# Kernel optimization log

Measured on AMD Instinct MI355X. Metric: run time of the kernel, lower is better.

Reference implementation:

```python
import jax, jax.numpy as jnp
import numpy as np

PI = np.pi


def _apply_1q(state, gate, wire, n):
    # state: [B, 2**n] complex64; gate: [2,2] (shared) or [B,2,2] (per-sample)
    # PennyLane convention: wire 0 is the most-significant bit of the state index.
    B = state.shape[0]
    left, right = 2 ** wire, 2 ** (n - wire - 1)
    s = state.reshape(B, left, 2, right)
    if gate.ndim == 2:
        s = jnp.einsum('kl,balr->bakr', gate, s)
    else:
        s = jnp.einsum('bkl,balr->bakr', gate, s)
    return s.reshape(B, -1)


def _apply_cz(state, wire, n):
    # CZ on (wire, wire+1): flip sign of |..11..> amplitudes
    B = state.shape[0]
    left, right = 2 ** wire, 2 ** (n - wire - 2)
    s = state.reshape(B, left, 2, 2, right)
    s = s.at[:, :, 1, 1, :].multiply(-1.0)
    return s.reshape(B, -1)


def _ry_batched(theta):
    # theta: [B] -> [B,2,2] complex RY(theta)
    h = 0.5 * theta
    c, s = jnp.cos(h), jnp.sin(h)
    g = jnp.stack([jnp.stack([c, -s], -1), jnp.stack([s, c], -1)], -2)
    return g.astype(jnp.complex64)


def _rot(phi, theta, omega):
    # Rot = RZ(omega) @ RY(theta) @ RZ(phi)
    c, s = jnp.cos(0.5 * theta), jnp.sin(0.5 * theta)
    e_mm = jnp.exp(-0.5j * (phi + omega))
    e_pm = jnp.exp(0.5j * (phi - omega))
    e_mp = jnp.exp(-0.5j * (phi - omega))
    e_pp = jnp.exp(0.5j * (phi + omega))
    g = jnp.stack([jnp.stack([e_mm * c, -e_pm * s]), jnp.stack([e_mp * s, e_pp * c])])
    return g.astype(jnp.complex64)


def _simulate(enc, weights):
    # enc: [B, n_qubits] in [-1,1]; weights: [n_layers, n_qubits, 3]
    n_layers, n, _ = weights.shape
    B = enc.shape[0]
    state = jnp.zeros((B, 2 ** n), jnp.complex64).at[:, 0].set(1.0)
    ry = [_ry_batched(enc[:, i] * PI) for i in range(n)]
    for l in range(n_layers):
        for i in range(n):
            state = _apply_1q(state, ry[i], i, n)
        for i in range(n):
            state = _apply_1q(state, _rot(weights[l, i, 0], weights[l, i, 1], weights[l, i, 2]), i, n)
        for i in range(n - 1):
            state = _apply_cz(state, i, n)
    for i in range(n):
        state = _apply_1q(state, ry[i], i, n)
    probs = state.real ** 2 + state.imag ** 2  # [B, 2**n]
    # <Z_i> = sum_k probs[k] * (-1)^bit_i(k), wire 0 = MSB
    bits = (jnp.arange(2 ** n)[None, :] >> (n - 1 - jnp.arange(n))[:, None]) & 1
    signs = (1 - 2 * bits).astype(probs.dtype)  # [n, 2**n]
    return probs @ signs.T  # [B, n]


def setup_inputs() -> dict:
    B, D, NQ, NL, NA = 32768, 16, 8, 4, 4
    key = jax.random.key(0)
    ks = jax.random.split(key, 6)

    def lin(k, o, i):
        b = 1.0 / np.sqrt(i)
        k1, k2 = jax.random.split(k)
        return (jax.random.uniform(k1, (o, i), jnp.float32, -b, b),
                jax.random.uniform(k2, (o,), jnp.float32, -b, b))

    enc_w1, enc_b1 = lin(ks[1], 8, D)
    enc_w2, enc_b2 = lin(ks[2], NQ, 8)
    dec_w1, dec_b1 = lin(ks[3], 8, NQ)
    dec_w2, dec_b2 = lin(ks[4], NA, 8)
    q_weights = jax.random.uniform(ks[5], (NL, NQ, 3), jnp.float32, 0.0, 2.0 * PI)
    x = jax.random.normal(ks[0], (B, D), jnp.float32)
    return {"x": x, "enc_w1": enc_w1, "enc_b1": enc_b1, "enc_w2": enc_w2, "enc_b2": enc_b2,
            "q_weights": q_weights, "dec_w1": dec_w1, "dec_b1": dec_b1, "dec_w2": dec_w2, "dec_b2": dec_b2}


def reference(x, enc_w1, enc_b1, enc_w2, enc_b2, q_weights, dec_w1, dec_b1, dec_w2, dec_b2):
    h = jax.nn.relu(x @ enc_w1.T + enc_b1)
    enc = jnp.tanh(h @ enc_w2.T + enc_b2)          # [B, n_qubits]
    q = _simulate(enc, q_weights)                  # [B, n_qubits] PauliZ expvals
    h2 = jax.nn.relu(q @ dec_w1.T + dec_b1)
    return h2 @ dec_w2.T + dec_b2                  # [B, n_actions]
```

## Files before the change

kernel.cpp:

```cpp
#include <hip/hip_runtime.h>
#include <math.h>


#define PI_F 3.14159265358979323846f

typedef float v2f __attribute__((ext_vector_type(2)));

struct C2 { float re, im; };
__device__ __forceinline__ C2 cmul(C2 a, C2 b) {
    C2 r;
    r.re = fmaf(a.re, b.re, -a.im * b.im);
    r.im = fmaf(a.re, b.im,  a.im * b.re);
    return r;
}
__device__ __forceinline__ float fxor(float x, int m) {
    return __int_as_float(__float_as_int(x) ^ m);
}

__device__ __forceinline__ v2f pk_mul(v2f a, v2f b) {
    v2f d; asm("v_pk_mul_f32 %0, %1, %2" : "=v"(d) : "v"(a), "v"(b)); return d;
}
__device__ __forceinline__ v2f pk_mul_neg(v2f a, v2f b) {
    v2f d; asm("v_pk_mul_f32 %0, %1, %2 neg_lo:[1,0] neg_hi:[1,0]"
               : "=v"(d) : "v"(a), "v"(b)); return d;
}
__device__ __forceinline__ v2f pk_fma(v2f a, v2f b, v2f c) {
    v2f d; asm("v_pk_fma_f32 %0, %1, %2, %3" : "=v"(d) : "v"(a), "v"(b), "v"(c)); return d;
}
__device__ __forceinline__ v2f pk_fma_nn(v2f a, v2f b, v2f c) {
    v2f d; asm("v_pk_fma_f32 %0, %1, %2, %3 neg_lo:[1,0,0] neg_hi:[1,0,0]"
               : "=v"(d) : "v"(a), "v"(b), "v"(c)); return d;
}
__device__ __forceinline__ v2f pk_fma_swl(v2f a, v2f b, v2f c) {
    v2f d; asm("v_pk_fma_f32 %0, %1, %2, %3 op_sel:[0,1,0] op_sel_hi:[1,0,1] neg_lo:[1,0,0]"
               : "=v"(d) : "v"(a), "v"(b), "v"(c)); return d;
}
__device__ __forceinline__ v2f pk_fma_swh(v2f a, v2f b, v2f c) {
    v2f d; asm("v_pk_fma_f32 %0, %1, %2, %3 op_sel:[0,1,0] op_sel_hi:[1,0,1] neg_hi:[1,0,0]"
               : "=v"(d) : "v"(a), "v"(b), "v"(c)); return d;
}
__device__ __forceinline__ v2f cmulv(v2f z, C2 c) {
    v2f n = pk_mul((v2f){c.re, c.re}, z);
    return pk_fma_swl((v2f){c.im, c.im}, z, n);
}

template<int CTRL>
__device__ __forceinline__ float dppf(float x) {
    int xi = __float_as_int(x);
    int r = __builtin_amdgcn_update_dpp(xi, xi, CTRL, 0xF, 0xF, false);
    return __int_as_float(r);
}
template<int M>
__device__ __forceinline__ float lxor(float x) {
    if constexpr (M == 1)      return dppf<0xB1>(x);
    else if constexpr (M == 2) return dppf<0x4E>(x);
    else                       return dppf<0x128>(x);
}

__device__ __forceinline__ void load_G2(const float* __restrict__ c_lds, int g,
                                        float cc, float ss,
                                        float& ar, float& ai, float& br, float& bi) {
    const float4 c0 = *(const float4*)(c_lds + 4 * g);
    ar = fmaf(c0.x, cc, -c0.z * ss);
    ai = fmaf(c0.y, cc,  c0.w * ss);
    br = fmaf(c0.z, cc,  c0.x * ss);
    bi = fmaf(c0.w, cc, -c0.y * ss);
}

template<int M>
__device__ __forceinline__ void su2_cross(v2f cSr, v2f cSi, v2f cOr, v2f cOi,
                                          v2f z[32]) {
#pragma unroll
    for (int c = 0; c < 4; c++) {
        v2f p[8];
#pragma unroll
        for (int k = 0; k < 8; k++) {
            p[k].x = lxor<M>(z[c * 8 + k].x);
            p[k].y = lxor<M>(z[c * 8 + k].y);
        }
#pragma unroll
        for (int k = 0; k < 8; k++) {
            const int t = c * 8 + k;
            v2f n = pk_mul(cSr, z[t]);
            n = pk_fma_swl(cSi, z[t], n);
            n = pk_fma   (cOr, p[k], n);
            n = pk_fma_swl(cOi, p[k], n);
            z[t] = n;
        }
    }
}

template<int ST>
__device__ __forceinline__ void su2_inlane(v2f arr, v2f aii, v2f brr, v2f bii,
                                           v2f z[32]) {
#pragma unroll
    for (int t = 0; t < 32; t++) {
        if ((t & ST) == 0) {
            const int u = t + ST;
            v2f x = z[t], y = z[u];
            v2f nx = pk_mul(arr, x);
            nx = pk_fma_swl(aii, x, nx);
            nx = pk_fma_nn (brr, y, nx);
            nx = pk_fma_swl(bii, y, nx);
            v2f ny = pk_mul(brr, x);
            ny = pk_fma_swl(bii, x, ny);
            ny = pk_fma   (arr, y, ny);
            ny = pk_fma_swh(aii, y, ny);
            z[t] = nx; z[u] = ny;
        }
    }
}

template<int M>
__device__ __forceinline__ void ry_cross(v2f cc, v2f cO, v2f z[32]) {
#pragma unroll
    for (int c = 0; c < 4; c++) {
        v2f p[8];
#pragma unroll
        for (int k = 0; k < 8; k++) {
            p[k].x = lxor<M>(z[c * 8 + k].x);
            p[k].y = lxor<M>(z[c * 8 + k].y);
        }
#pragma unroll
        for (int k = 0; k < 8; k++) {
            const int t = c * 8 + k;
            z[t] = pk_fma(cO, p[k], pk_mul(cc, z[t]));
        }
    }
}
template<int ST>
__device__ __forceinline__ void ry_inlane(v2f cc, v2f ss, v2f z[32]) {
#pragma unroll
    for (int t = 0; t < 32; t++) {
        if ((t & ST) == 0) {
            const int u = t + ST;
            v2f x = z[t], y = z[u];
            z[t] = pk_fma_nn(ss, y, pk_mul(cc, x));
            z[u] = pk_fma   (cc, y, pk_mul(ss, x));
        }
    }
}

__host__ __device__ constexpr bool czt5(int t) {
    return ((((t >> 4) & (t >> 3)) ^ ((t >> 3) & (t >> 2)) ^
             ((t >> 2) & (t >> 1)) ^ ((t >> 1) & t)) & 1) != 0;
}

__global__ __launch_bounds__(128, 2) void qdqn_kernel(
    const float* __restrict__ x,
    const float* __restrict__ ew1, const float* __restrict__ eb1,
    const float* __restrict__ ew2, const float* __restrict__ eb2,
    const float* __restrict__ qw,
    const float* __restrict__ dw1, const float* __restrict__ db1,
    const float* __restrict__ dw2, const float* __restrict__ db2,
    float* __restrict__ out, int B, int NL) {
    __shared__ __align__(16) float c_lds[32 * 4];
    __shared__ __align__(16) float hx[2][8][8];
    __shared__ __align__(16) float csx[2][8][16];

    const int tid = threadIdx.x;
    const int wave = tid >> 6;
    const int lane = tid & 63;
    const int g = (lane & 3) | ((lane >> 1) & 4);
    const int grp = ((lane >> 2) & 1) | ((lane >> 3) & 6);
    int s = blockIdx.x * 16 + wave * 8 + grp;
    if (s >= B) s = B - 1;

    float xv[16];
    {
        const float4* xp = (const float4*)(x + s * 16);
#pragma unroll
        for (int i = 0; i < 4; i++) {
            float4 v = xp[i];
            xv[4*i] = v.x; xv[4*i+1] = v.y; xv[4*i+2] = v.z; xv[4*i+3] = v.w;
        }
    }

    const int n_gates = NL * 8;
    if (tid < n_gates) {
        const int gg = tid;
        float phi = qw[3 * gg + 0], th = qw[3 * gg + 1], om = qw[3 * gg + 2];
        float c = __cosf(0.5f * th), sv = __sinf(0.5f * th);
        float A = 0.5f * (phi + om), Bb = 0.5f * (phi - om);
        float* o = c_lds + 4 * gg;
        o[0] =  __cosf(A) * c;   o[1] = -__sinf(A) * c;
        o[2] =  __cosf(Bb) * sv; o[3] = -__sinf(Bb) * sv;
    }
    __syncthreads();

    float cq[8], sq[8];
    {
        float a = eb1[g];
#pragma unroll
        for (int i = 0; i < 16; i++) a = fmaf(ew1[g * 16 + i], xv[i], a);
        hx[wave][grp][g] = fmaxf(a, 0.0f);
        __builtin_amdgcn_wave_barrier();
        float4 h01 = *(const float4*)&hx[wave][grp][0];
        float4 h23 = *(const float4*)&hx[wave][grp][4];
        float b = eb2[g];
        b = fmaf(ew2[g*8+0], h01.x, b); b = fmaf(ew2[g*8+1], h01.y, b);
        b = fmaf(ew2[g*8+2], h01.z, b); b = fmaf(ew2[g*8+3], h01.w, b);
        b = fmaf(ew2[g*8+4], h23.x, b); b = fmaf(ew2[g*8+5], h23.y, b);
        b = fmaf(ew2[g*8+6], h23.z, b); b = fmaf(ew2[g*8+7], h23.w, b);
        float e = 1.0f - __fdividef(2.0f, __expf(2.0f * b) + 1.0f);
        float ang = e * (0.5f * PI_F);
        float2* cso = (float2*)&csx[wave][grp][2 * g];
        *cso = make_float2(__cosf(ang), __sinf(ang));
        __builtin_amdgcn_wave_barrier();
#pragma unroll
        for (int k = 0; k < 4; k++) {
            float4 v = *(const float4*)&csx[wave][grp][4 * k];
            cq[2*k] = v.x; sq[2*k] = v.y; cq[2*k+1] = v.z; sq[2*k+1] = v.w;
        }
    }

    int hiM[3], loM[3];
#pragma unroll
    for (int q = 0; q < 3; q++) {
        int hi = (g >> (2 - q)) & 1;
        hiM[q] = hi << 31;
        loM[q] = hiM[q] ^ 0x80000000;
    }

    const int g0b = g & 1, g1b = (g >> 1) & 1, g2b = (g >> 2) & 1;
    const float mLo = ((g2b & g1b) ^ (g1b & g0b)) ? -1.0f : 1.0f;
    const float mHi = g0b ? -mLo : mLo;
    const v2f mLo2 = (v2f){mLo, mLo}, mHi2 = (v2f){mHi, mHi};

    v2f z[32];
    {
        C2 P; P.re = 1.0f; P.im = 0.0f;
        C2 A[5], Bc[5];
#pragma unroll
        for (int q = 0; q < 8; q++) {
            float ar, ai, br, bi;
            load_G2(c_lds, q, cq[q], sq[q], ar, ai, br, bi);
            if (q < 3) {
                const bool hi = (g >> (2 - q)) & 1;
                C2 f; f.re = hi ? br : ar; f.im = hi ? bi : ai;
                P = cmul(P, f);
            } else {
                A[q-3].re = ar;  A[q-3].im = ai;
                Bc[q-3].re = br; Bc[q-3].im = bi;
            }
        }
        z[0] = (v2f){P.re, P.im};
#pragma unroll
        for (int w = 0; w < 5; w++) {
            const int n = 1 << w;
#pragma unroll
            for (int i = n - 1; i >= 0; i--) {
                v2f v = z[i];
                z[2*i+1] = cmulv(v, Bc[w]);
                z[2*i]   = cmulv(v, A[w]);
            }
        }
#pragma unroll
        for (int t = 0; t < 32; t++) {
            v2f m = (t < 16) ? mLo2 : mHi2;
            z[t] = czt5(t) ? pk_mul_neg(m, z[t]) : pk_mul(m, z[t]);
        }
    }

    for (int l = 1; l < NL; l++) {
        const int gb = l * 8;
        float ar, ai, br, bi;
        load_G2(c_lds, gb+0, cq[0], sq[0], ar, ai, br, bi);
        su2_cross<8>((v2f){ar,ar}, (v2f){fxor(ai,hiM[0]),fxor(ai,hiM[0])},
                     (v2f){fxor(br,loM[0]),fxor(br,loM[0])}, (v2f){bi,bi}, z);
        load_G2(c_lds, gb+1, cq[1], sq[1], ar, ai, br, bi);
        su2_cross<2>((v2f){ar,ar}, (v2f){fxor(ai,hiM[1]),fxor(ai,hiM[1])},
                     (v2f){fxor(br,loM[1]),fxor(br,loM[1])}, (v2f){bi,bi}, z);
        load_G2(c_lds, gb+2, cq[2], sq[2], ar, ai, br, bi);
        su2_cross<1>((v2f){ar,ar}, (v2f){fxor(ai,hiM[2]),fxor(ai,hiM[2])},
                     (v2f){fxor(br,loM[2]),fxor(br,loM[2])}, (v2f){bi,bi}, z);
        load_G2(c_lds, gb+3, cq[3], sq[3], ar, ai, br, bi);
        su2_inlane<16>((v2f){ar,ar}, (v2f){ai,ai}, (v2f){br,br}, (v2f){bi,bi}, z);
        load_G2(c_lds, gb+4, cq[4], sq[4], ar, ai, br, bi);
        su2_inlane<8>((v2f){ar,ar}, (v2f){ai,ai}, (v2f){br,br}, (v2f){bi,bi}, z);
        load_G2(c_lds, gb+5, cq[5], sq[5], ar, ai, br, bi);
        su2_inlane<4>((v2f){ar,ar}, (v2f){ai,ai}, (v2f){br,br}, (v2f){bi,bi}, z);
        load_G2(c_lds, gb+6, cq[6], sq[6], ar, ai, br, bi);
        su2_inlane<2>((v2f){ar,ar}, (v2f){ai,ai}, (v2f){br,br}, (v2f){bi,bi}, z);
        load_G2(c_lds, gb+7, cq[7], sq[7], ar, ai, br, bi);
        su2_inlane<1>((v2f){ar,ar}, (v2f){ai,ai}, (v2f){br,br}, (v2f){bi,bi}, z);
#pragma unroll
        for (int t = 0; t < 32; t++) {
            v2f m = (t < 16) ? mLo2 : mHi2;
            z[t] = czt5(t) ? pk_mul_neg(m, z[t]) : pk_mul(m, z[t]);
        }
    }

    {
        v2f cc, cO, ss;
        cc=(v2f){cq[0],cq[0]}; cO=(v2f){fxor(sq[0],loM[0]),fxor(sq[0],loM[0])};
        ry_cross<8>(cc, cO, z);
        cc=(v2f){cq[1],cq[1]}; cO=(v2f){fxor(sq[1],loM[1]),fxor(sq[1],loM[1])};
        ry_cross<2>(cc, cO, z);
        cc=(v2f){cq[2],cq[2]}; cO=(v2f){fxor(sq[2],loM[2]),fxor(sq[2],loM[2])};
        ry_cross<1>(cc, cO, z);
        cc=(v2f){cq[3],cq[3]}; ss=(v2f){sq[3],sq[3]}; ry_inlane<16>(cc, ss, z);
        cc=(v2f){cq[4],cq[4]}; ss=(v2f){sq[4],sq[4]}; ry_inlane<8>(cc, ss, z);
        cc=(v2f){cq[5],cq[5]}; ss=(v2f){sq[5],sq[5]}; ry_inlane<4>(cc, ss, z);
        cc=(v2f){cq[6],cq[6]}; ss=(v2f){sq[6],sq[6]}; ry_inlane<2>(cc, ss, z);
        cc=(v2f){cq[7],cq[7]}; ss=(v2f){sq[7],sq[7]}; ry_inlane<1>(cc, ss, z);
    }

    float p[32];
#pragma unroll
    for (int t = 0; t < 32; t++) p[t] = fmaf(z[t].x, z[t].x, z[t].y * z[t].y);

    float s16[16], zW[8];
    {
        float d = 0.0f;
#pragma unroll
        for (int i = 0; i < 16; i++) {
            s16[i] = p[2*i] + p[2*i+1];
            d += p[2*i] - p[2*i+1];
        }
        zW[7] = d;
        float s8[8]; d = 0.0f;
#pragma unroll
        for (int i = 0; i < 8; i++) {
            s8[i] = s16[2*i] + s16[2*i+1];
            d += s16[2*i] - s16[2*i+1];
        }
        zW[6] = d;
        float s4[4]; d = 0.0f;
#pragma unroll
        for (int i = 0; i < 4; i++) {
            s4[i] = s8[2*i] + s8[2*i+1];
            d += s8[2*i] - s8[2*i+1];
        }
        zW[5] = d;
        float s2a = s4[0] + s4[1], s2b = s4[2] + s4[3];
        zW[4] = (s4[0] - s4[1]) + (s4[2] - s4[3]);
        float sumP = s2a + s2b;
        zW[3] = s2a - s2b;
        zW[0] = g2b ? -sumP : sumP;
        zW[1] = g1b ? -sumP : sumP;
        zW[2] = g0b ? -sumP : sumP;
    }
#pragma unroll
    for (int w = 0; w < 8; w++) zW[w] += lxor<1>(zW[w]);
#pragma unroll
    for (int w = 0; w < 8; w++) zW[w] += lxor<2>(zW[w]);
#pragma unroll
    for (int w = 0; w < 8; w++) zW[w] += lxor<8>(zW[w]);

    {
        float a = db1[g];
#pragma unroll
        for (int w = 0; w < 8; w++) a = fmaf(dw1[g * 8 + w], zW[w], a);
        hx[wave][grp][g] = fmaxf(a, 0.0f);
        __builtin_amdgcn_wave_barrier();
        float4 h01 = *(const float4*)&hx[wave][grp][0];
        float4 h23 = *(const float4*)&hx[wave][grp][4];
        const int o = g & 3;
        float acc = db2[o];
        acc = fmaf(dw2[o*8+0], h01.x, acc); acc = fmaf(dw2[o*8+1], h01.y, acc);
        acc = fmaf(dw2[o*8+2], h01.z, acc); acc = fmaf(dw2[o*8+3], h01.w, acc);
        acc = fmaf(dw2[o*8+4], h23.x, acc); acc = fmaf(dw2[o*8+5], h23.y, acc);
        acc = fmaf(dw2[o*8+6], h23.z, acc); acc = fmaf(dw2[o*8+7], h23.w, acc);
        out[s * 4 + o] = acc;
    }
}

extern "C" void kernel_launch(void* const* d_in, const int* in_sizes, int n_in,
                              void* d_out, int out_size, void* d_ws, size_t ws_size,
                              hipStream_t stream) {
    const float* x   = (const float*)d_in[0];
    const float* ew1 = (const float*)d_in[1];
    const float* eb1 = (const float*)d_in[2];
    const float* ew2 = (const float*)d_in[3];
    const float* eb2 = (const float*)d_in[4];
    const float* qw  = (const float*)d_in[5];
    const float* dw1 = (const float*)d_in[6];
    const float* db1 = (const float*)d_in[7];
    const float* dw2 = (const float*)d_in[8];
    const float* db2 = (const float*)d_in[9];
    float* out = (float*)d_out;

    int B = in_sizes[0] / 16;
    int n_gates = in_sizes[5] / 3;
    int NL = n_gates / 8;

    int blocks = (B + 15) / 16;
    qdqn_kernel<<<blocks, 128, 0, stream>>>(x, ew1, eb1, ew2, eb2, qw,
                                            dw1, db1, dw2, db2, out, B, NL);
}
```

Baseline: 117.1 us.

## Spread each sample's state over 16 lanes with 16 amplitudes per lane

Each sample's 256-amplitude statevector now lives on 16 lanes holding 16 complex amplitudes each, instead of 8 lanes holding 32. Four qubits become cross-lane (one new qubit uses ds_swizzle) and four stay in-lane. The block grows to 256 threads so each block still covers 16 samples. This halves per-thread register pressure to raise occupancy (launch bounds 256,6), at the cost of more cross-lane shuffles and an LDS swizzle with higher latency than DPP.

```diff
diff --git a/kernel.cpp b/kernel.cpp
--- a/kernel.cpp
+++ b/kernel.cpp
@@ -54,6 +54,8 @@
 __device__ __forceinline__ float lxor(float x) {
     if constexpr (M == 1)      return dppf<0xB1>(x);
     else if constexpr (M == 2) return dppf<0x4E>(x);
+    else if constexpr (M == 4) return __int_as_float(
+        __builtin_amdgcn_ds_swizzle(__float_as_int(x), 0x101F));
     else                       return dppf<0x128>(x);
 }
 
@@ -69,9 +71,9 @@
 
 template<int M>
 __device__ __forceinline__ void su2_cross(v2f cSr, v2f cSi, v2f cOr, v2f cOi,
-                                          v2f z[32]) {
-#pragma unroll
-    for (int c = 0; c < 4; c++) {
+                                          v2f z[16]) {
+#pragma unroll
+    for (int c = 0; c < 2; c++) {
         v2f p[8];
 #pragma unroll
         for (int k = 0; k < 8; k++) {
@@ -92,9 +94,9 @@
 
 template<int ST>
 __device__ __forceinline__ void su2_inlane(v2f arr, v2f aii, v2f brr, v2f bii,
-                                           v2f z[32]) {
-#pragma unroll
-    for (int t = 0; t < 32; t++) {
+                                           v2f z[16]) {
+#pragma unroll
+    for (int t = 0; t < 16; t++) {
         if ((t & ST) == 0) {
             const int u = t + ST;
             v2f x = z[t], y = z[u];
@@ -112,9 +114,9 @@
 }
 
 template<int M>
-__device__ __forceinline__ void ry_cross(v2f cc, v2f cO, v2f z[32]) {
-#pragma unroll
-    for (int c = 0; c < 4; c++) {
+__device__ __forceinline__ void ry_cross(v2f cc, v2f cO, v2f z[16]) {
+#pragma unroll
+    for (int c = 0; c < 2; c++) {
         v2f p[8];
 #pragma unroll
         for (int k = 0; k < 8; k++) {
@@ -129,9 +131,9 @@
     }
 }
 template<int ST>
-__device__ __forceinline__ void ry_inlane(v2f cc, v2f ss, v2f z[32]) {
-#pragma unroll
-    for (int t = 0; t < 32; t++) {
+__device__ __forceinline__ void ry_inlane(v2f cc, v2f ss, v2f z[16]) {
+#pragma unroll
+    for (int t = 0; t < 16; t++) {
         if ((t & ST) == 0) {
             const int u = t + ST;
             v2f x = z[t], y = z[u];
@@ -141,12 +143,11 @@
     }
 }
 
-__host__ __device__ constexpr bool czt5(int t) {
-    return ((((t >> 4) & (t >> 3)) ^ ((t >> 3) & (t >> 2)) ^
-             ((t >> 2) & (t >> 1)) ^ ((t >> 1) & t)) & 1) != 0;
-}
-
-__global__ __launch_bounds__(128, 2) void qdqn_kernel(
+__host__ __device__ constexpr bool czt4(int t) {
+    return ((((t >> 3) & (t >> 2)) ^ ((t >> 2) & (t >> 1)) ^ ((t >> 1) & t)) & 1) != 0;
+}
+
+__global__ __launch_bounds__(256, 6) void qdqn_kernel(
     const float* __restrict__ x,
     const float* __restrict__ ew1, const float* __restrict__ eb1,
     const float* __restrict__ ew2, const float* __restrict__ eb2,
@@ -155,15 +156,15 @@
     const float* __restrict__ dw2, const float* __restrict__ db2,
     float* __restrict__ out, int B, int NL) {
     __shared__ __align__(16) float c_lds[32 * 4];
-    __shared__ __align__(16) float hx[2][8][8];
-    __shared__ __align__(16) float csx[2][8][16];
+    __shared__ __align__(16) float hx[4][4][8];
+    __shared__ __align__(16) float csx[4][4][16];
 
     const int tid = threadIdx.x;
     const int wave = tid >> 6;
     const int lane = tid & 63;
-    const int g = (lane & 3) | ((lane >> 1) & 4);
-    const int grp = ((lane >> 2) & 1) | ((lane >> 3) & 6);
-    int s = blockIdx.x * 16 + wave * 8 + grp;
+    const int grp = lane >> 4;
+    const int L = lane & 15;
+    int s = blockIdx.x * 16 + wave * 4 + grp;
     if (s >= B) s = B - 1;
 
     float xv[16];
@@ -190,22 +191,25 @@
 
     float cq[8], sq[8];
     {
-        float a = eb1[g];
-#pragma unroll
-        for (int i = 0; i < 16; i++) a = fmaf(ew1[g * 16 + i], xv[i], a);
-        hx[wave][grp][g] = fmaxf(a, 0.0f);
+        const int r = L & 7;
+        float a = eb1[r];
+#pragma unroll
+        for (int i = 0; i < 16; i++) a = fmaf(ew1[r * 16 + i], xv[i], a);
+        if (L < 8) hx[wave][grp][r] = fmaxf(a, 0.0f);
         __builtin_amdgcn_wave_barrier();
         float4 h01 = *(const float4*)&hx[wave][grp][0];
         float4 h23 = *(const float4*)&hx[wave][grp][4];
-        float b = eb2[g];
-        b = fmaf(ew2[g*8+0], h01.x, b); b = fmaf(ew2[g*8+1], h01.y, b);
-        b = fmaf(ew2[g*8+2], h01.z, b); b = fmaf(ew2[g*8+3], h01.w, b);
-        b = fmaf(ew2[g*8+4], h23.x, b); b = fmaf(ew2[g*8+5], h23.y, b);
-        b = fmaf(ew2[g*8+6], h23.z, b); b = fmaf(ew2[g*8+7], h23.w, b);
+        float b = eb2[r];
+        b = fmaf(ew2[r*8+0], h01.x, b); b = fmaf(ew2[r*8+1], h01.y, b);
+        b = fmaf(ew2[r*8+2], h01.z, b); b = fmaf(ew2[r*8+3], h01.w, b);
+        b = fmaf(ew2[r*8+4], h23.x, b); b = fmaf(ew2[r*8+5], h23.y, b);
+        b = fmaf(ew2[r*8+6], h23.z, b); b = fmaf(ew2[r*8+7], h23.w, b);
         float e = 1.0f - __fdividef(2.0f, __expf(2.0f * b) + 1.0f);
         float ang = e * (0.5f * PI_F);
-        float2* cso = (float2*)&csx[wave][grp][2 * g];
-        *cso = make_float2(__cosf(ang), __sinf(ang));
+        if (L < 8) {
+            float2* cso = (float2*)&csx[wave][grp][2 * r];
+            *cso = make_float2(__cosf(ang), __sinf(ang));
+        }
         __builtin_amdgcn_wave_barrier();
 #pragma unroll
         for (int k = 0; k < 4; k++) {
@@ -214,51 +218,52 @@
         }
     }
 
-    int hiM[3], loM[3];
-#pragma unroll
-    for (int q = 0; q < 3; q++) {
-        int hi = (g >> (2 - q)) & 1;
+    int hiM[4], loM[4];
+#pragma unroll
+    for (int q = 0; q < 4; q++) {
+        int hi = (L >> (3 - q)) & 1;
         hiM[q] = hi << 31;
         loM[q] = hiM[q] ^ 0x80000000;
     }
 
-    const int g0b = g & 1, g1b = (g >> 1) & 1, g2b = (g >> 2) & 1;
-    const float mLo = ((g2b & g1b) ^ (g1b & g0b)) ? -1.0f : 1.0f;
-    const float mHi = g0b ? -mLo : mLo;
-    const v2f mLo2 = (v2f){mLo, mLo}, mHi2 = (v2f){mHi, mHi};
-
-    v2f z[32];
+    const int L0 = L & 1, L1b = (L >> 1) & 1, L2b = (L >> 2) & 1, L3b = (L >> 3) & 1;
+    const int cnt = (L3b & L2b) ^ (L2b & L1b) ^ (L1b & L0);
+    const float mL = cnt ? -1.0f : 1.0f;
+    const float mH = L0 ? -mL : mL;
+    const v2f mL2 = (v2f){mL, mL}, mH2 = (v2f){mH, mH};
+
+    v2f z[16];
     {
         C2 P; P.re = 1.0f; P.im = 0.0f;
-        C2 A[5], Bc[5];
+        C2 F[4][2];
 #pragma unroll
         for (int q = 0; q < 8; q++) {
             float ar, ai, br, bi;
             load_G2(c_lds, q, cq[q], sq[q], ar, ai, br, bi);
-            if (q < 3) {
-                const bool hi = (g >> (2 - q)) & 1;
+            if (q < 4) {
+                const bool hi = (L >> (3 - q)) & 1;
                 C2 f; f.re = hi ? br : ar; f.im = hi ? bi : ai;
                 P = cmul(P, f);
             } else {
-                A[q-3].re = ar;  A[q-3].im = ai;
-                Bc[q-3].re = br; Bc[q-3].im = bi;
+                F[q-4][0].re = ar; F[q-4][0].im = ai;
+                F[q-4][1].re = br; F[q-4][1].im = bi;
             }
         }
         z[0] = (v2f){P.re, P.im};
 #pragma unroll
-        for (int w = 0; w < 5; w++) {
+        for (int w = 0; w < 4; w++) {
             const int n = 1 << w;
 #pragma unroll
             for (int i = n - 1; i >= 0; i--) {
                 v2f v = z[i];
-                z[2*i+1] = cmulv(v, Bc[w]);
-                z[2*i]   = cmulv(v, A[w]);
+                z[2*i+1] = cmulv(v, F[w][1]);
+                z[2*i]   = cmulv(v, F[w][0]);
             }
         }
 #pragma unroll
-        for (int t = 0; t < 32; t++) {
-            v2f m = (t < 16) ? mLo2 : mHi2;
-            z[t] = czt5(t) ? pk_mul_neg(m, z[t]) : pk_mul(m, z[t]);
+        for (int t = 0; t < 16; t++) {
+            v2f m = (t < 8) ? mL2 : mH2;
+            z[t] = czt4(t) ? pk_mul_neg(m, z[t]) : pk_mul(m, z[t]);
         }
     }
 
@@ -269,13 +274,14 @@
         su2_cross<8>((v2f){ar,ar}, (v2f){fxor(ai,hiM[0]),fxor(ai,hiM[0])},
                      (v2f){fxor(br,loM[0]),fxor(br,loM[0])}, (v2f){bi,bi}, z);
         load_G2(c_lds, gb+1, cq[1], sq[1], ar, ai, br, bi);
-        su2_cross<2>((v2f){ar,ar}, (v2f){fxor(ai,hiM[1]),fxor(ai,hiM[1])},
+        su2_cross<4>((v2f){ar,ar}, (v2f){fxor(ai,hiM[1]),fxor(ai,hiM[1])},
                      (v2f){fxor(br,loM[1]),fxor(br,loM[1])}, (v2f){bi,bi}, z);
         load_G2(c_lds, gb+2, cq[2], sq[2], ar, ai, br, bi);
-        su2_cross<1>((v2f){ar,ar}, (v2f){fxor(ai,hiM[2]),fxor(ai,hiM[2])},
+        su2_cross<2>((v2f){ar,ar}, (v2f){fxor(ai,hiM[2]),fxor(ai,hiM[2])},
                      (v2f){fxor(br,loM[2]),fxor(br,loM[2])}, (v2f){bi,bi}, z);
         load_G2(c_lds, gb+3, cq[3], sq[3], ar, ai, br, bi);
-        su2_inlane<16>((v2f){ar,ar}, (v2f){ai,ai}, (v2f){br,br}, (v2f){bi,bi}, z);
+        su2_cross<1>((v2f){ar,ar}, (v2f){fxor(ai,hiM[3]),fxor(ai,hiM[3])},
+                     (v2f){fxor(br,loM[3]),fxor(br,loM[3])}, (v2f){bi,bi}, z);
         load_G2(c_lds, gb+4, cq[4], sq[4], ar, ai, br, bi);
         su2_inlane<8>((v2f){ar,ar}, (v2f){ai,ai}, (v2f){br,br}, (v2f){bi,bi}, z);
         load_G2(c_lds, gb+5, cq[5], sq[5], ar, ai, br, bi);
@@ -285,9 +291,9 @@
         load_G2(c_lds, gb+7, cq[7], sq[7], ar, ai, br, bi);
         su2_inlane<1>((v2f){ar,ar}, (v2f){ai,ai}, (v2f){br,br}, (v2f){bi,bi}, z);
 #pragma unroll
-        for (int t = 0; t < 32; t++) {
-            v2f m = (t < 16) ? mLo2 : mHi2;
-            z[t] = czt5(t) ? pk_mul_neg(m, z[t]) : pk_mul(m, z[t]);
+        for (int t = 0; t < 16; t++) {
+            v2f m = (t < 8) ? mL2 : mH2;
+            z[t] = czt4(t) ? pk_mul_neg(m, z[t]) : pk_mul(m, z[t]);
         }
     }
 
@@ -296,73 +302,64 @@
         cc=(v2f){cq[0],cq[0]}; cO=(v2f){fxor(sq[0],loM[0]),fxor(sq[0],loM[0])};
         ry_cross<8>(cc, cO, z);
         cc=(v2f){cq[1],cq[1]}; cO=(v2f){fxor(sq[1],loM[1]),fxor(sq[1],loM[1])};
+        ry_cross<4>(cc, cO, z);
+        cc=(v2f){cq[2],cq[2]}; cO=(v2f){fxor(sq[2],loM[2]),fxor(sq[2],loM[2])};
         ry_cross<2>(cc, cO, z);
-        cc=(v2f){cq[2],cq[2]}; cO=(v2f){fxor(sq[2],loM[2]),fxor(sq[2],loM[2])};
+        cc=(v2f){cq[3],cq[3]}; cO=(v2f){fxor(sq[3],loM[3]),fxor(sq[3],loM[3])};
         ry_cross<1>(cc, cO, z);
-        cc=(v2f){cq[3],cq[3]}; ss=(v2f){sq[3],sq[3]}; ry_inlane<16>(cc, ss, z);
         cc=(v2f){cq[4],cq[4]}; ss=(v2f){sq[4],sq[4]}; ry_inlane<8>(cc, ss, z);
         cc=(v2f){cq[5],cq[5]}; ss=(v2f){sq[5],sq[5]}; ry_inlane<4>(cc, ss, z);
         cc=(v2f){cq[6],cq[6]}; ss=(v2f){sq[6],sq[6]}; ry_inlane<2>(cc, ss, z);
         cc=(v2f){cq[7],cq[7]}; ss=(v2f){sq[7],sq[7]}; ry_inlane<1>(cc, ss, z);
     }
 
-    float p[32];
-#pragma unroll
-    for (int t = 0; t < 32; t++) p[t] = fmaf(z[t].x, z[t].x, z[t].y * z[t].y);
-
-    float s16[16], zW[8];
-    {
-        float d = 0.0f;
-#pragma unroll
-        for (int i = 0; i < 16; i++) {
-            s16[i] = p[2*i] + p[2*i+1];
-            d += p[2*i] - p[2*i+1];
-        }
-        zW[7] = d;
-        float s8[8]; d = 0.0f;
-#pragma unroll
-        for (int i = 0; i < 8; i++) {
-            s8[i] = s16[2*i] + s16[2*i+1];
-            d += s16[2*i] - s16[2*i+1];
-        }
-        zW[6] = d;
-        float s4[4]; d = 0.0f;
-#pragma unroll
-        for (int i = 0; i < 4; i++) {
-            s4[i] = s8[2*i] + s8[2*i+1];
-            d += s8[2*i] - s8[2*i+1];
-        }
-        zW[5] = d;
-        float s2a = s4[0] + s4[1], s2b = s4[2] + s4[3];
-        zW[4] = (s4[0] - s4[1]) + (s4[2] - s4[3]);
-        float sumP = s2a + s2b;
-        zW[3] = s2a - s2b;
-        zW[0] = g2b ? -sumP : sumP;
-        zW[1] = g1b ? -sumP : sumP;
-        zW[2] = g0b ? -sumP : sumP;
-    }
+    float p[16];
+#pragma unroll
+    for (int t = 0; t < 16; t++) p[t] = fmaf(z[t].x, z[t].x, z[t].y * z[t].y);
+
+    float e0 = p[0]+p[1],  e1 = p[2]+p[3],  e2 = p[4]+p[5],  e3 = p[6]+p[7];
+    float e4 = p[8]+p[9],  e5 = p[10]+p[11], e6 = p[12]+p[13], e7 = p[14]+p[15];
+    float q0 = e0+e1, q1 = e2+e3, q2 = e4+e5, q3 = e6+e7;
+    float h0 = q0+q1, h1 = q2+q3;
+    float sumP = h0 + h1;
+
+    float zW[8];
+    zW[0] = L3b ? -sumP : sumP;
+    zW[1] = L2b ? -sumP : sumP;
+    zW[2] = L1b ? -sumP : sumP;
+    zW[3] = L0  ? -sumP : sumP;
+    zW[4] = h0 - h1;
+    zW[5] = (q0 - q1) + (q2 - q3);
+    zW[6] = (e0 - e1) + (e2 - e3) + (e4 - e5) + (e6 - e7);
+    zW[7] = (p[0]-p[1]) + (p[2]-p[3]) + (p[4]-p[5]) + (p[6]-p[7])
+          + (p[8]-p[9]) + (p[10]-p[11]) + (p[12]-p[13]) + (p[14]-p[15]);
+
 #pragma unroll
     for (int w = 0; w < 8; w++) zW[w] += lxor<1>(zW[w]);
 #pragma unroll
     for (int w = 0; w < 8; w++) zW[w] += lxor<2>(zW[w]);
 #pragma unroll
+    for (int w = 0; w < 8; w++) zW[w] += lxor<4>(zW[w]);
+#pragma unroll
     for (int w = 0; w < 8; w++) zW[w] += lxor<8>(zW[w]);
 
     {
-        float a = db1[g];
-#pragma unroll
-        for (int w = 0; w < 8; w++) a = fmaf(dw1[g * 8 + w], zW[w], a);
-        hx[wave][grp][g] = fmaxf(a, 0.0f);
+        const int r = L & 7;
+        float a = db1[r];
+#pragma unroll
+        for (int w = 0; w < 8; w++) a = fmaf(dw1[r * 8 + w], zW[w], a);
+        if (L < 8) hx[wave][grp][r] = fmaxf(a, 0.0f);
         __builtin_amdgcn_wave_barrier();
-        float4 h01 = *(const float4*)&hx[wave][grp][0];
-        float4 h23 = *(const float4*)&hx[wave][grp][4];
-        const int o = g & 3;
-        float acc = db2[o];
-        acc = fmaf(dw2[o*8+0], h01.x, acc); acc = fmaf(dw2[o*8+1], h01.y, acc);
-        acc = fmaf(dw2[o*8+2], h01.z, acc); acc = fmaf(dw2[o*8+3], h01.w, acc);
-        acc = fmaf(dw2[o*8+4], h23.x, acc); acc = fmaf(dw2[o*8+5], h23.y, acc);
-        acc = fmaf(dw2[o*8+6], h23.z, acc); acc = fmaf(dw2[o*8+7], h23.w, acc);
-        out[s * 4 + o] = acc;
+        if (L < 4) {
+            float4 h01 = *(const float4*)&hx[wave][grp][0];
+            float4 h23 = *(const float4*)&hx[wave][grp][4];
+            float acc = db2[L];
+            acc = fmaf(dw2[L*8+0], h01.x, acc); acc = fmaf(dw2[L*8+1], h01.y, acc);
+            acc = fmaf(dw2[L*8+2], h01.z, acc); acc = fmaf(dw2[L*8+3], h01.w, acc);
+            acc = fmaf(dw2[L*8+4], h23.x, acc); acc = fmaf(dw2[L*8+5], h23.y, acc);
+            acc = fmaf(dw2[L*8+6], h23.z, acc); acc = fmaf(dw2[L*8+7], h23.w, acc);
+            out[s * 4 + L] = acc;
+        }
     }
 }
 
@@ -386,6 +383,6 @@
     int NL = n_gates / 8;
 
     int blocks = (B + 15) / 16;
-    qdqn_kernel<<<blocks, 128, 0, stream>>>(x, ew1, eb1, ew2, eb2, qw,
+    qdqn_kernel<<<blocks, 256, 0, stream>>>(x, ew1, eb1, ew2, eb2, qw,
                                             dw1, db1, dw2, db2, out, B, NL);
 }
```

Result: slower. 130.7 us (+11.6%).
